# Kernel tuning notes

Hardware: AMD Instinct MI355X
Metric: run time of the kernel (lower is better)

## Reference

```python
import jax, jax.numpy as jnp
import numpy as np

N = 50000        # nodes
E = 1600000      # edges
G = 512          # graphs in batch
IN = 128         # in_dim
HID = 32         # hidden_dim
H = 4            # heads in conv1
NEG_SLOPE = 0.2  # PyG GATConv default


def setup_inputs() -> dict:
    key = jax.random.key(0)
    ks = jax.random.split(key, 20)
    s = 0.05
    return {
        "x": jax.random.normal(ks[0], (N, IN), jnp.float32),
        "edge_index": jax.random.randint(ks[1], (2, E), 0, N, dtype=jnp.int64),
        "edge_attr": jax.random.normal(ks[2], (E, 8), jnp.float32),
        "batch": jnp.sort(jax.random.randint(ks[3], (N,), 0, G, dtype=jnp.int64)),
        # conv1: in=IN, out=HID, heads=H, concat=True
        "W1": jax.random.normal(ks[4], (IN, H * HID), jnp.float32) * s,
        "a_src1": jax.random.normal(ks[5], (H, HID), jnp.float32) * s,
        "a_dst1": jax.random.normal(ks[6], (H, HID), jnp.float32) * s,
        "b1": jnp.zeros((H * HID,), jnp.float32),
        # conv2: in=H*HID, out=HID, heads=1, concat=False
        "W2": jax.random.normal(ks[7], (H * HID, HID), jnp.float32) * s,
        "a_src2": jax.random.normal(ks[8], (1, HID), jnp.float32) * s,
        "a_dst2": jax.random.normal(ks[9], (1, HID), jnp.float32) * s,
        "b2": jnp.zeros((HID,), jnp.float32),
        # classifier: HID -> HID//2 -> 1
        "Wc1": jax.random.normal(ks[10], (HID, HID // 2), jnp.float32) * s,
        "bc1": jnp.zeros((HID // 2,), jnp.float32),
        "Wc2": jax.random.normal(ks[11], (HID // 2, 1), jnp.float32) * s,
        "bc2": jnp.zeros((1,), jnp.float32),
    }


def gat_layer(x, src, dst, W, a_src, a_dst, b, heads, ch, concat, n):
    """PyG GATConv (eval mode): linear, edge-gathered additive attention,
    per-destination segment softmax, scatter-add aggregation."""
    h = (x @ W).reshape(n, heads, ch)                       # [N,H,C]
    alpha_s = jnp.sum(h * a_src, axis=-1)                   # [N,H]
    alpha_d = jnp.sum(h * a_dst, axis=-1)                   # [N,H]
    e = jax.nn.leaky_relu(alpha_s[src] + alpha_d[dst], NEG_SLOPE)  # [Etot,H]
    m = jax.lax.stop_gradient(jax.ops.segment_max(e, dst, num_segments=n))
    ex = jnp.exp(e - m[dst])
    den = jax.ops.segment_sum(ex, dst, num_segments=n)      # [N,H]
    alpha = ex / den[dst]                                   # [Etot,H]
    out = jax.ops.segment_sum(alpha[:, :, None] * h[src], dst, num_segments=n)
    out = out.reshape(n, heads * ch) if concat else out.mean(axis=1)
    return out + b


def reference(x, edge_index, edge_attr, batch,
              W1, a_src1, a_dst1, b1,
              W2, a_src2, a_dst2, b2,
              Wc1, bc1, Wc2, bc2):
    # add self-loops (PyG GATConv default)
    loop = jnp.arange(N, dtype=edge_index.dtype)
    src = jnp.concatenate([edge_index[0], loop])
    dst = jnp.concatenate([edge_index[1], loop])

    h = jax.nn.elu(gat_layer(x, src, dst, W1, a_src1, a_dst1, b1, H, HID, True, N))
    h = jax.nn.elu(gat_layer(h, src, dst, W2, a_src2, a_dst2, b2, 1, HID, False, N))

    # global mean pool over graphs
    cnt = jax.ops.segment_sum(jnp.ones((N,), h.dtype), batch, num_segments=G)
    pooled = jax.ops.segment_sum(h, batch, num_segments=G) / cnt[:, None]

    z = jax.nn.relu(pooled @ Wc1 + bc1)
    return (z @ Wc2 + bc2).squeeze(-1)   # [G]
```

## Files before the change

### kernel.cpp

```cpp
#include <hip/hip_runtime.h>
#include <math.h>

#define BUCKET_SHIFT 7
#define BUCKET_NODES (1 << BUCKET_SHIFT)
#define MAX_BUCK 512
#define PART_CHUNK 8192
#define PART_EPT 32

typedef _Float16 half4v __attribute__((ext_vector_type(4)));
typedef _Float16 half8v __attribute__((ext_vector_type(8)));

__device__ __forceinline__ float leaky02(float x){ return x > 0.f ? x : 0.2f * x; }
__device__ __forceinline__ float eluf(float x){ return x > 0.f ? x : expm1f(x); }

__global__ __launch_bounds__(128) void gemm1_kernel(
    const float* __restrict__ x, const float* __restrict__ W,
    const float* __restrict__ a_src, const float* __restrict__ a_dst,
    _Float16* __restrict__ h, float* __restrict__ as_, float* __restrict__ ad_, int n)
{
  const int t = threadIdx.x;
  const int row0 = blockIdx.x * 8;
  __shared__ float xs[8][128];
  __shared__ float sS[8][128];
  __shared__ float sD[8][128];
  for (int idx = t; idx < 8 * 32; idx += 128) {
    int r = idx >> 5, k4 = idx & 31;
    float4 v = (row0 + r < n) ? ((const float4*)x)[(size_t)(row0 + r) * 32 + k4]
                              : make_float4(0.f, 0.f, 0.f, 0.f);
    *(float4*)&xs[r][k4 * 4] = v;
  }
  __syncthreads();
  float acc[8] = {0,0,0,0,0,0,0,0};
  for (int k = 0; k < 128; k += 4) {
    float w0 = W[(k + 0) * 128 + t];
    float w1 = W[(k + 1) * 128 + t];
    float w2 = W[(k + 2) * 128 + t];
    float w3 = W[(k + 3) * 128 + t];
    #pragma unroll
    for (int r = 0; r < 8; ++r) {
      float4 xv = *(const float4*)&xs[r][k];
      acc[r] += xv.x * w0 + xv.y * w1 + xv.z * w2 + xv.w * w3;
    }
  }
  float asv = a_src[t], adv = a_dst[t];
  #pragma unroll
  for (int r = 0; r < 8; ++r) {
    float hv = acc[r];
    if (row0 + r < n) h[(size_t)(row0 + r) * 128 + t] = (_Float16)hv;
    sS[r][t] = hv * asv;
    sD[r][t] = hv * adv;
  }
  __syncthreads();
  if (t < 64) {
    int r = t >> 3, head = t & 3, which = (t >> 2) & 1;
    if (row0 + r < n) {
      const float (*buf)[128] = which ? sD : sS;
      double s = 0;
      for (int cc = 0; cc < 32; ++cc) s += (double)buf[r][head * 32 + cc];
      float* dstp = which ? ad_ : as_;
      dstp[(row0 + r) * 4 + head] = (float)s;
    }
  }
}

__global__ __launch_bounds__(128) void gemm2_kernel(
    const _Float16* __restrict__ x, const float* __restrict__ W,
    const float* __restrict__ a_src, const float* __restrict__ a_dst,
    _Float16* __restrict__ h, float* __restrict__ as_, float* __restrict__ ad_, int n)
{
  const int t = threadIdx.x;
  const int row0 = blockIdx.x * 8;
  __shared__ float xs[8][128];
  __shared__ float sH[8][32];
  for (int idx = t; idx < 8 * 16; idx += 128) {
    int r = idx >> 4, k8 = idx & 15;
    half8v v;
    #pragma unroll
    for (int q = 0; q < 8; ++q) v[q] = (_Float16)0.f;
    if (row0 + r < n) v = ((const half8v*)x)[(size_t)(row0 + r) * 16 + k8];
    #pragma unroll
    for (int q = 0; q < 8; ++q) xs[r][k8 * 8 + q] = (float)v[q];
  }
  __syncthreads();
  int col = t & 31, rp = t >> 5;
  int r0 = rp * 2, r1 = r0 + 1;
  float a0 = 0, a1 = 0;
  for (int k = 0; k < 128; k += 4) {
    float w0 = W[(k + 0) * 32 + col];
    float w1 = W[(k + 1) * 32 + col];
    float w2 = W[(k + 2) * 32 + col];
    float w3 = W[(k + 3) * 32 + col];
    float4 x0 = *(const float4*)&xs[r0][k];
    float4 x1 = *(const float4*)&xs[r1][k];
    a0 += x0.x * w0 + x0.y * w1 + x0.z * w2 + x0.w * w3;
    a1 += x1.x * w0 + x1.y * w1 + x1.z * w2 + x1.w * w3;
  }
  if (row0 + r0 < n) h[(size_t)(row0 + r0) * 32 + col] = (_Float16)a0;
  if (row0 + r1 < n) h[(size_t)(row0 + r1) * 32 + col] = (_Float16)a1;
  sH[r0][col] = a0; sH[r1][col] = a1;
  __syncthreads();
  if (t < 16) {
    int r = t >> 1, which = t & 1;
    if (row0 + r < n) {
      const float* a = which ? a_dst : a_src;
      double s = 0;
      for (int cc = 0; cc < 32; ++cc) s += (double)sH[r][cc] * (double)a[cc];
      (which ? ad_ : as_)[row0 + r] = (float)s;
    }
  }
}

__global__ __launch_bounds__(256) void bucket_hist_kernel(
    const int* __restrict__ dst, int* __restrict__ bucketCount, int E, int K)
{
  __shared__ int hist[MAX_BUCK];
  for (int b = threadIdx.x; b < K; b += 256) hist[b] = 0;
  __syncthreads();
  int cbase = blockIdx.x * PART_CHUNK;
  for (int j = 0; j < PART_EPT; ++j) {
    int e = cbase + j * 256 + threadIdx.x;
    if (e < E) atomicAdd(&hist[dst[e] >> BUCKET_SHIFT], 1);
  }
  __syncthreads();
  for (int b = threadIdx.x; b < K; b += 256)
    if (hist[b]) atomicAdd(&bucketCount[b], hist[b]);
}

__global__ __launch_bounds__(256) void partition_kernel(
    const int* __restrict__ src, const int* __restrict__ dst,
    const int* __restrict__ bucketStart, int* __restrict__ cursorB,
    int2* __restrict__ bucketed, int E, int K)
{
  __shared__ int hist[MAX_BUCK];
  __shared__ int base_s[MAX_BUCK];
  __shared__ int cur[MAX_BUCK];
  for (int b = threadIdx.x; b < K; b += 256) hist[b] = 0;
  __syncthreads();
  int cbase = blockIdx.x * PART_CHUNK;
  for (int j = 0; j < PART_EPT; ++j) {
    int e = cbase + j * 256 + threadIdx.x;
    if (e < E) atomicAdd(&hist[dst[e] >> BUCKET_SHIFT], 1);
  }
  __syncthreads();
  for (int b = threadIdx.x; b < K; b += 256) {
    int c = hist[b];
    base_s[b] = c ? bucketStart[b] + atomicAdd(&cursorB[b], c) : 0;
    cur[b] = 0;
  }
  __syncthreads();
  for (int j = 0; j < PART_EPT; ++j) {
    int e = cbase + j * 256 + threadIdx.x;
    if (e < E) {
      int d = dst[e];
      int b = d >> BUCKET_SHIFT;
      int r = atomicAdd(&cur[b], 1);
      bucketed[base_s[b] + r] = make_int2(src[e], d);
    }
  }
}

__global__ __launch_bounds__(256) void fill_csr_kernel(
    const int2* __restrict__ bucketed, const int* __restrict__ bucketStart,
    int* __restrict__ rowStart, int* __restrict__ col, int n, int E, int K)
{
  int b = blockIdx.x;
  int nodeBase = b << BUCKET_SHIFT;
  int t = threadIdx.x;
  __shared__ int hist[BUCKET_NODES];
  __shared__ int rs[BUCKET_NODES];
  __shared__ int cur[BUCKET_NODES];
  if (t < BUCKET_NODES) hist[t] = 0;
  __syncthreads();
  int bs = bucketStart[b];
  int be = (b + 1 < K) ? bucketStart[b + 1] : E;
  for (int i = bs + t; i < be; i += 256)
    atomicAdd(&hist[bucketed[i].y - nodeBase], 1);
  __syncthreads();
  if (t < BUCKET_NODES) rs[t] = hist[t];
  __syncthreads();
  for (int off = 1; off < BUCKET_NODES; off <<= 1) {
    int v = (t < BUCKET_NODES && t >= off) ? rs[t - off] : 0;
    __syncthreads();
    if (t < BUCKET_NODES) rs[t] += v;
    __syncthreads();
  }
  if (t < BUCKET_NODES) {
    int node = nodeBase + t;
    int excl = bs + rs[t] - hist[t];
    if (node < n) rowStart[node] = excl;
    rs[t] = excl;
    cur[t] = 0;
  }
  if (b == K - 1 && t == 0) rowStart[n] = E;
  __syncthreads();
  for (int i = bs + t; i < be; i += 256) {
    int2 rec = bucketed[i];
    int local = rec.y - nodeBase;
    int pos = rs[local] + atomicAdd(&cur[local], 1);
    col[pos] = rec.x;
  }
}

__global__ __launch_bounds__(256) void gat_aggr_w16_kernel(
    const _Float16* __restrict__ feat,
    const float* __restrict__ as_,
    const float* __restrict__ ad_,
    const int* __restrict__ rowStart,
    const int* __restrict__ col,
    const float* __restrict__ bias,
    _Float16* __restrict__ out, int n)
{
  constexpr int L    = 16;
  constexpr int NPW  = 4;
  constexpr int NPB  = 16;
  constexpr int CHUNK = 16;

  const int t    = threadIdx.x;
  const int wave = t >> 6;
  const int lane = t & 63;
  const int grp  = lane >> 4;
  const int li   = lane & 15;
  const int slot = wave * NPW + grp;
  const int node = blockIdx.x * NPB + slot;
  const int hc   = li >> 2;

  __shared__ int   s_off[NPB][CHUNK + 1];
  __shared__ float s_p[NPB][CHUNK * 4 + 1];

  if (node >= n) return;

  const int beg = rowStart[node];
  const int deg = rowStart[node + 1] - beg;

  const float4 advv = ((const float4*)ad_)[node];
  const float4 asvv = ((const float4*)as_)[node];
  float adv[4] = {advv.x, advv.y, advv.z, advv.w};
  float eself[4];
  eself[0] = leaky02(asvv.x + adv[0]);
  eself[1] = leaky02(asvv.y + adv[1]);
  eself[2] = leaky02(asvv.z + adv[2]);
  eself[3] = leaky02(asvv.w + adv[3]);
  float es = 0.f;
  #pragma unroll
  for (int h = 0; h < 4; ++h) if (h == hc) es = eself[h];
  const float ps = expf(es);

  const char* featc = (const char*)feat + (li << 4);
  const half8v fself = *(const half8v*)(featc + ((size_t)node << 8));
  double acc64[8];
  #pragma unroll
  for (int q = 0; q < 8; ++q) acc64[q] = (double)ps * (double)(float)fself[q];
  double den64 = (double)ps;

  for (int base = 0; base < deg; base += CHUNK) {
    const int cnt = min(CHUNK, deg - base);
    if (li < cnt) {
      int s = col[beg + base + li];
      s_off[slot][li] = s << 8;
      float4 q = ((const float4*)as_)[s];
      s_p[slot][li * 4 + 0] = expf(leaky02(q.x + adv[0]));
      s_p[slot][li * 4 + 1] = expf(leaky02(q.y + adv[1]));
      s_p[slot][li * 4 + 2] = expf(leaky02(q.z + adv[2]));
      s_p[slot][li * 4 + 3] = expf(leaky02(q.w + adv[3]));
    }
    __builtin_amdgcn_wave_barrier();
    float a[8] = {0,0,0,0,0,0,0,0};
    float df = 0.f;
    #pragma unroll 4
    for (int j = 0; j < cnt; ++j) {
      int boff = s_off[slot][j];
      float p = s_p[slot][j * 4 + hc];
      const half8v f = *(const half8v*)(featc + boff);
      #pragma unroll
      for (int q = 0; q < 8; ++q) a[q] += p * (float)f[q];
      df += p;
    }
    __builtin_amdgcn_wave_barrier();
    #pragma unroll
    for (int q = 0; q < 8; ++q) acc64[q] += a[q];
    den64 += df;
  }

  const float4 bv0 = ((const float4*)bias)[2 * li];
  const float4 bv1 = ((const float4*)bias)[2 * li + 1];
  const float bb[8] = {bv0.x, bv0.y, bv0.z, bv0.w, bv1.x, bv1.y, bv1.z, bv1.w};
  const double inv = 1.0 / den64;
  half8v ov;
  #pragma unroll
  for (int q = 0; q < 8; ++q)
    ov[q] = (_Float16)eluf((float)(acc64[q] * inv) + bb[q]);
  *(half8v*)((char*)out + ((size_t)node << 8) + (li << 4)) = ov;
}

template<int CTOT, int H>
__global__ __launch_bounds__(256) void gat_aggr3_kernel(
    const _Float16* __restrict__ feat,
    const float* __restrict__ as_,
    const float* __restrict__ ad_,
    const int* __restrict__ rowStart,
    const int* __restrict__ col,
    const float* __restrict__ bias,
    float* __restrict__ out, int n)
{
  constexpr int L    = CTOT / 4;
  constexpr int NPW  = 64 / L;
  constexpr int NPB  = 4 * NPW;
  constexpr int CH   = CTOT / H;
  constexpr int CHUNK = L;

  const int t    = threadIdx.x;
  const int wave = t >> 6;
  const int lane = t & 63;
  const int grp  = lane / L;
  const int li   = lane % L;
  const int slot = wave * NPW + grp;
  const int node = blockIdx.x * NPB + slot;
  const int hc   = (4 * li) / CH;

  __shared__ int   s_off[NPB][CHUNK + 1];
  __shared__ float s_p[NPB][CHUNK * H + 1];

  if (node >= n) return;

  const int beg = rowStart[node];
  const int deg = rowStart[node + 1] - beg;

  float adv[H], eself[H];
  #pragma unroll
  for (int h = 0; h < H; ++h) adv[h] = ad_[node * H + h];
  #pragma unroll
  for (int h = 0; h < H; ++h) eself[h] = leaky02(as_[node * H + h] + adv[h]);

  float es = 0.f;
  #pragma unroll
  for (int h = 0; h < H; ++h) if (h == hc) es = eself[h];
  const float ps = expf(es);

  const half4v fself = *(const half4v*)(feat + (size_t)node * CTOT + 4 * li);
  double acc64[4];
  acc64[0] = (double)ps * (double)(float)fself.x;
  acc64[1] = (double)ps * (double)(float)fself.y;
  acc64[2] = (double)ps * (double)(float)fself.z;
  acc64[3] = (double)ps * (double)(float)fself.w;
  double den64 = (double)ps;

  for (int base = 0; base < deg; base += CHUNK) {
    const int cnt = min(CHUNK, deg - base);
    if (li < cnt) {
      int s = col[beg + base + li];
      s_off[slot][li] = s * CTOT;
      if constexpr (H == 4) {
        float4 q = ((const float4*)as_)[s];
        s_p[slot][li * 4 + 0] = expf(leaky02(q.x + adv[0]));
        s_p[slot][li * 4 + 1] = expf(leaky02(q.y + adv[1]));
        s_p[slot][li * 4 + 2] = expf(leaky02(q.z + adv[2]));
        s_p[slot][li * 4 + 3] = expf(leaky02(q.w + adv[3]));
      } else {
        s_p[slot][li] = expf(leaky02(as_[s] + adv[0]));
      }
    }
    __builtin_amdgcn_wave_barrier();
    float a0 = 0.f, a1 = 0.f, a2 = 0.f, a3 = 0.f, df = 0.f;
    #pragma unroll 8
    for (int j = 0; j < cnt; ++j) {
      int off = s_off[slot][j];
      float p = (H == 4) ? s_p[slot][j * 4 + hc] : s_p[slot][j];
      const half4v f = *(const half4v*)(feat + off + 4 * li);
      a0 += p * (float)f.x; a1 += p * (float)f.y;
      a2 += p * (float)f.z; a3 += p * (float)f.w;
      df += p;
    }
    __builtin_amdgcn_wave_barrier();
    acc64[0] += a0; acc64[1] += a1; acc64[2] += a2; acc64[3] += a3;
    den64 += df;
  }

  const float4 bv = *(const float4*)(bias + 4 * li);
  float4 o;
  o.x = eluf((float)(acc64[0] / den64) + bv.x);
  o.y = eluf((float)(acc64[1] / den64) + bv.y);
  o.z = eluf((float)(acc64[2] / den64) + bv.z);
  o.w = eluf((float)(acc64[3] / den64) + bv.w);
  *(float4*)(out + (size_t)node * CTOT + 4 * li) = o;
}

__global__ __launch_bounds__(256) void pool_kernel(const float* __restrict__ act2,
    const int* __restrict__ batch, float* __restrict__ pooled,
    float* __restrict__ cnt, int n)
{
  int t = threadIdx.x;
  int c = t & 31, r = t >> 5;
  int n0 = blockIdx.x * 64 + r * 8;
  float run = 0.f; int gcur = -1; int len = 0;
  for (int i = 0; i < 8; ++i) {
    int nd = n0 + i;
    if (nd >= n) break;
    int gb = batch[nd];
    if (gb != gcur) {
      if (gcur >= 0) {
        atomicAdd(&pooled[gcur * 32 + c], run);
        if (c == 0) atomicAdd(&cnt[gcur], (float)len);
      }
      gcur = gb; run = 0.f; len = 0;
    }
    run += act2[(size_t)nd * 32 + c];
    len++;
  }
  if (gcur >= 0) {
    atomicAdd(&pooled[gcur * 32 + c], run);
    if (c == 0) atomicAdd(&cnt[gcur], (float)len);
  }
}

__global__ void classifier_kernel(const float* __restrict__ pooled, const float* __restrict__ cnt,
    const float* __restrict__ Wc1, const float* __restrict__ bc1,
    const float* __restrict__ Wc2, const float* __restrict__ bc2,
    float* __restrict__ outp, int g_total)
{
  int g = blockIdx.x * blockDim.x + threadIdx.x;
  if (g < g_total) {
    float inv = 1.0f / cnt[g];
    float pm[32];
    for (int c = 0; c < 32; ++c) pm[c] = pooled[g * 32 + c] * inv;
    double o = (double)bc2[0];
    for (int j = 0; j < 16; ++j) {
      double z = (double)bc1[j];
      for (int c = 0; c < 32; ++c) z += (double)pm[c] * (double)Wc1[c * 16 + j];
      float zr = (float)z;
      zr = zr > 0.f ? zr : 0.f;
      o += (double)zr * (double)Wc2[j];
    }
    outp[g] = (float)o;
  }
}

extern "C" void kernel_launch(void* const* d_in, const int* in_sizes, int n_in,
                              void* d_out, int out_size, void* d_ws, size_t ws_size,
                              hipStream_t stream)
{
  const float* x      = (const float*)d_in[0];
  const int*   ei     = (const int*)d_in[1];
  const int*   batch  = (const int*)d_in[3];
  const float* W1     = (const float*)d_in[4];
  const float* a_src1 = (const float*)d_in[5];
  const float* a_dst1 = (const float*)d_in[6];
  const float* b1     = (const float*)d_in[7];
  const float* W2     = (const float*)d_in[8];
  const float* a_src2 = (const float*)d_in[9];
  const float* a_dst2 = (const float*)d_in[10];
  const float* b2     = (const float*)d_in[11];
  const float* Wc1    = (const float*)d_in[12];
  const float* bc1    = (const float*)d_in[13];
  const float* Wc2    = (const float*)d_in[14];
  const float* bc2    = (const float*)d_in[15];

  const int N = in_sizes[0] / 128;
  const int E = in_sizes[1] / 2;
  const int G = out_size;

  const int* srcv = ei;
  const int* dstv = ei + E;

  char* ws = (char*)d_ws;
  size_t off = 0;
  auto alloc = [&](size_t bytes) -> void* {
    void* p = ws + off;
    off += (bytes + 255) & ~(size_t)255;
    return p;
  };
  _Float16* h1   = (_Float16*)alloc((size_t)N * 128 * 2);
  _Float16* act1 = (_Float16*)alloc((size_t)N * 128 * 2);
  _Float16* h2   = (_Float16*)alloc((size_t)N * 32 * 2);
  float* act2  = (float*)alloc((size_t)N * 32 * 4);
  float* as1   = (float*)alloc((size_t)N * 4 * 4);
  float* ad1   = (float*)alloc((size_t)N * 4 * 4);
  float* as2   = (float*)alloc((size_t)N * 4);
  float* ad2   = (float*)alloc((size_t)N * 4);
  int*   rowStart = (int*)alloc((size_t)(N + 1) * 4);
  int*   colv     = (int*)alloc((size_t)E * 4);
  int*   bucketCount = (int*)alloc((size_t)MAX_BUCK * 4);
  int*   cursorB     = (int*)alloc((size_t)MAX_BUCK * 4);
  int2*  bucketed    = (int2*)alloc((size_t)E * 8);
  float* pooled   = (float*)alloc((size_t)G * 32 * 4);
  float* cntG     = (float*)alloc((size_t)G * 4);

  const int K = (N + BUCKET_NODES - 1) >> BUCKET_SHIFT;

  hipMemsetAsync(bucketCount, 0, (size_t)K * 4, stream);
  hipMemsetAsync(cursorB,     0, (size_t)K * 4, stream);
  hipMemsetAsync(pooled, 0, (size_t)G * 32 * 4, stream);
  hipMemsetAsync(cntG,   0, (size_t)G * 4, stream);

  int pb = (E + PART_CHUNK - 1) / PART_CHUNK;
  bucket_hist_kernel<<<pb, 256, 0, stream>>>(dstv, bucketCount, E, K);
  {
    extern __global__ void scan_offsets_kernel(int*, int);
  }
  void(0);
  {
    extern const int __dummy;
  }
  extern __global__ void scan_offsets_kernel(int* __restrict__, int);
  scan_offsets_kernel<<<1, 256, 0, stream>>>(bucketCount, K);
  partition_kernel<<<pb, 256, 0, stream>>>(srcv, dstv, bucketCount, cursorB, bucketed, E, K);
  fill_csr_kernel<<<K, 256, 0, stream>>>(bucketed, bucketCount, rowStart, colv, N, E, K);

  gemm1_kernel<<<(N + 7) / 8, 128, 0, stream>>>(x, W1, a_src1, a_dst1, h1, as1, ad1, N);
  gat_aggr_w16_kernel<<<(N + 15) / 16, 256, 0, stream>>>(h1, as1, ad1, rowStart, colv, b1, act1, N);

  gemm2_kernel<<<(N + 7) / 8, 128, 0, stream>>>(act1, W2, a_src2, a_dst2, h2, as2, ad2, N);
  gat_aggr3_kernel<32, 1><<<(N + 31) / 32, 256, 0, stream>>>(h2, as2, ad2, rowStart, colv, b2, act2, N);

  pool_kernel<<<(N + 63) / 64, 256, 0, stream>>>(act2, batch, pooled, cntG, N);
  classifier_kernel<<<(G + 255) / 256, 256, 0, stream>>>(pooled, cntG, Wc1, bc1, Wc2, bc2,
                                                         (float*)d_out, G);
}

__global__ __launch_bounds__(256) void scan_offsets_kernel(int* __restrict__ partial, int nb) {
  __shared__ int s[256];
  __shared__ int carry_s;
  int t = threadIdx.x;
  if (t == 0) carry_s = 0;
  __syncthreads();
  for (int b = 0; b < nb; b += 256) {
    int v = (b + t < nb) ? partial[b + t] : 0;
    s[t] = v;
    __syncthreads();
    for (int off = 1; off < 256; off <<= 1) {
      int x = (t >= off) ? s[t - off] : 0;
      __syncthreads();
      s[t] += x;
      __syncthreads();
    }
    int incl = s[t];
    int carry = carry_s;
    if (b + t < nb) partial[b + t] = carry + incl - v;
    __syncthreads();
    if (t == 255) carry_s = carry + incl;
    __syncthreads();
  }
}
```

Measured before the change: 398.3 us.

## Fuse setup launches, pack bucketed edges, prefetch and batch gathers in aggregation

Four memsets are replaced by zeroing inside gemm1's first block. The offset scan is folded into bucket_hist through a last-block-done counter, and the classifier is folded into the pool kernel the same way. Bucketed edge records shrink from int2 to one packed 32-bit word (src<<7 | local dst), which halves the partition and fill traffic. Both aggregation kernels now prefetch the next chunk's column indices and source scores one chunk ahead, and issue all 16 feature gathers before accumulating. Risks are the ordering assumption that gemm1 finishes zeroing before bucket_hist starts (same stream), higher register pressure from 16 outstanding loads, and the packed encoding requiring src < 2^25.

```diff
diff --git a/kernel.cpp b/kernel.cpp
--- a/kernel.cpp
+++ b/kernel.cpp
@@ -16,9 +16,13 @@
 __global__ __launch_bounds__(128) void gemm1_kernel(
     const float* __restrict__ x, const float* __restrict__ W,
     const float* __restrict__ a_src, const float* __restrict__ a_dst,
-    _Float16* __restrict__ h, float* __restrict__ as_, float* __restrict__ ad_, int n)
+    _Float16* __restrict__ h, float* __restrict__ as_, float* __restrict__ ad_, int n,
+    int* __restrict__ zbase, int zwords)
 {
   const int t = threadIdx.x;
+  if (blockIdx.x == 0) {
+    for (int i = t; i < zwords; i += 128) zbase[i] = 0;
+  }
   const int row0 = blockIdx.x * 8;
   __shared__ float xs[8][128];
   __shared__ float sS[8][128];
@@ -111,25 +115,53 @@
 }
 
 __global__ __launch_bounds__(256) void bucket_hist_kernel(
-    const int* __restrict__ dst, int* __restrict__ bucketCount, int E, int K)
+    const int* __restrict__ dst, int* __restrict__ bucketCount,
+    int* __restrict__ doneCtr, int E, int K)
 {
   __shared__ int hist[MAX_BUCK];
-  for (int b = threadIdx.x; b < K; b += 256) hist[b] = 0;
+  const int t = threadIdx.x;
+  for (int b = t; b < K; b += 256) hist[b] = 0;
   __syncthreads();
   int cbase = blockIdx.x * PART_CHUNK;
   for (int j = 0; j < PART_EPT; ++j) {
-    int e = cbase + j * 256 + threadIdx.x;
+    int e = cbase + j * 256 + t;
     if (e < E) atomicAdd(&hist[dst[e] >> BUCKET_SHIFT], 1);
   }
   __syncthreads();
-  for (int b = threadIdx.x; b < K; b += 256)
+  for (int b = t; b < K; b += 256)
     if (hist[b]) atomicAdd(&bucketCount[b], hist[b]);
+  __threadfence();
+  __shared__ unsigned int tick;
+  if (t == 0) tick = atomicAdd((unsigned int*)doneCtr, 1u);
+  __syncthreads();
+  if (tick != gridDim.x - 1) return;
+  __shared__ int s[256];
+  __shared__ int carry_s;
+  if (t == 0) carry_s = 0;
+  __syncthreads();
+  for (int b = 0; b < K; b += 256) {
+    int v = (b + t < K) ? atomicAdd(&bucketCount[b + t], 0) : 0;
+    s[t] = v;
+    __syncthreads();
+    for (int off = 1; off < 256; off <<= 1) {
+      int x = (t >= off) ? s[t - off] : 0;
+      __syncthreads();
+      s[t] += x;
+      __syncthreads();
+    }
+    int incl = s[t];
+    int carry = carry_s;
+    if (b + t < K) bucketCount[b + t] = carry + incl - v;
+    __syncthreads();
+    if (t == 255) carry_s = carry + incl;
+    __syncthreads();
+  }
 }
 
 __global__ __launch_bounds__(256) void partition_kernel(
     const int* __restrict__ src, const int* __restrict__ dst,
     const int* __restrict__ bucketStart, int* __restrict__ cursorB,
-    int2* __restrict__ bucketed, int E, int K)
+    unsigned int* __restrict__ bucketed, int E, int K)
 {
   __shared__ int hist[MAX_BUCK];
   __shared__ int base_s[MAX_BUCK];
@@ -154,13 +186,14 @@
       int d = dst[e];
       int b = d >> BUCKET_SHIFT;
       int r = atomicAdd(&cur[b], 1);
-      bucketed[base_s[b] + r] = make_int2(src[e], d);
+      bucketed[base_s[b] + r] =
+          ((unsigned int)src[e] << BUCKET_SHIFT) | (unsigned int)(d & (BUCKET_NODES - 1));
     }
   }
 }
 
 __global__ __launch_bounds__(256) void fill_csr_kernel(
-    const int2* __restrict__ bucketed, const int* __restrict__ bucketStart,
+    const unsigned int* __restrict__ bucketed, const int* __restrict__ bucketStart,
     int* __restrict__ rowStart, int* __restrict__ col, int n, int E, int K)
 {
   int b = blockIdx.x;
@@ -174,7 +207,7 @@
   int bs = bucketStart[b];
   int be = (b + 1 < K) ? bucketStart[b + 1] : E;
   for (int i = bs + t; i < be; i += 256)
-    atomicAdd(&hist[bucketed[i].y - nodeBase], 1);
+    atomicAdd(&hist[bucketed[i] & (BUCKET_NODES - 1)], 1);
   __syncthreads();
   if (t < BUCKET_NODES) rs[t] = hist[t];
   __syncthreads();
@@ -194,14 +227,14 @@
   if (b == K - 1 && t == 0) rowStart[n] = E;
   __syncthreads();
   for (int i = bs + t; i < be; i += 256) {
-    int2 rec = bucketed[i];
-    int local = rec.y - nodeBase;
+    unsigned int rec = bucketed[i];
+    int local = rec & (BUCKET_NODES - 1);
     int pos = rs[local] + atomicAdd(&cur[local], 1);
-    col[pos] = rec.x;
-  }
-}
-
-__global__ __launch_bounds__(256) void gat_aggr_w16_kernel(
+    col[pos] = (int)(rec >> BUCKET_SHIFT);
+  }
+}
+
+__global__ __launch_bounds__(256) void gat_aggr1_kernel(
     const _Float16* __restrict__ feat,
     const float* __restrict__ as_,
     const float* __restrict__ ad_,
@@ -210,22 +243,18 @@
     const float* __restrict__ bias,
     _Float16* __restrict__ out, int n)
 {
-  constexpr int L    = 16;
-  constexpr int NPW  = 4;
-  constexpr int NPB  = 16;
   constexpr int CHUNK = 16;
-
   const int t    = threadIdx.x;
   const int wave = t >> 6;
   const int lane = t & 63;
   const int grp  = lane >> 4;
   const int li   = lane & 15;
-  const int slot = wave * NPW + grp;
-  const int node = blockIdx.x * NPB + slot;
+  const int slot = wave * 4 + grp;
+  const int node = blockIdx.x * 16 + slot;
   const int hc   = li >> 2;
 
-  __shared__ int   s_off[NPB][CHUNK + 1];
-  __shared__ float s_p[NPB][CHUNK * 4 + 1];
+  __shared__ int   s_off[16][CHUNK];
+  __shared__ float s_p[16][CHUNK * 4];
 
   if (node >= n) return;
 
@@ -234,15 +263,15 @@
 
   const float4 advv = ((const float4*)ad_)[node];
   const float4 asvv = ((const float4*)as_)[node];
-  float adv[4] = {advv.x, advv.y, advv.z, advv.w};
-  float eself[4];
-  eself[0] = leaky02(asvv.x + adv[0]);
-  eself[1] = leaky02(asvv.y + adv[1]);
-  eself[2] = leaky02(asvv.z + adv[2]);
-  eself[3] = leaky02(asvv.w + adv[3]);
-  float es = 0.f;
-  #pragma unroll
-  for (int h = 0; h < 4; ++h) if (h == hc) es = eself[h];
+  const float adv[4] = {advv.x, advv.y, advv.z, advv.w};
+  float es;
+  {
+    float e0 = leaky02(asvv.x + adv[0]);
+    float e1 = leaky02(asvv.y + adv[1]);
+    float e2 = leaky02(asvv.z + adv[2]);
+    float e3 = leaky02(asvv.w + adv[3]);
+    es = (hc == 0) ? e0 : (hc == 1) ? e1 : (hc == 2) ? e2 : e3;
+  }
   const float ps = expf(es);
 
   const char* featc = (const char*)feat + (li << 4);
@@ -252,28 +281,57 @@
   for (int q = 0; q < 8; ++q) acc64[q] = (double)ps * (double)(float)fself[q];
   double den64 = (double)ps;
 
-  for (int base = 0; base < deg; base += CHUNK) {
-    const int cnt = min(CHUNK, deg - base);
+  int    st_s = 0;
+  float4 st_q = make_float4(0.f, 0.f, 0.f, 0.f);
+  if (deg > 0 && li < min(CHUNK, deg)) {
+    st_s = col[beg + li];
+    st_q = ((const float4*)as_)[st_s];
+  }
+
+  const int nch = (deg + CHUNK - 1) / CHUNK;
+  for (int c = 0; c < nch; ++c) {
+    const int base = c * CHUNK;
+    const int cnt  = min(CHUNK, deg - base);
     if (li < cnt) {
-      int s = col[beg + base + li];
-      s_off[slot][li] = s << 8;
-      float4 q = ((const float4*)as_)[s];
-      s_p[slot][li * 4 + 0] = expf(leaky02(q.x + adv[0]));
-      s_p[slot][li * 4 + 1] = expf(leaky02(q.y + adv[1]));
-      s_p[slot][li * 4 + 2] = expf(leaky02(q.z + adv[2]));
-      s_p[slot][li * 4 + 3] = expf(leaky02(q.w + adv[3]));
+      s_off[slot][li] = st_s << 8;
+      float4 pp;
+      pp.x = expf(leaky02(st_q.x + adv[0]));
+      pp.y = expf(leaky02(st_q.y + adv[1]));
+      pp.z = expf(leaky02(st_q.z + adv[2]));
+      pp.w = expf(leaky02(st_q.w + adv[3]));
+      *(float4*)&s_p[slot][li * 4] = pp;
     }
     __builtin_amdgcn_wave_barrier();
+    const int nbase = base + CHUNK;
+    if (nbase + li < deg) {
+      st_s = col[beg + nbase + li];
+      st_q = ((const float4*)as_)[st_s];
+    }
     float a[8] = {0,0,0,0,0,0,0,0};
     float df = 0.f;
-    #pragma unroll 4
-    for (int j = 0; j < cnt; ++j) {
-      int boff = s_off[slot][j];
-      float p = s_p[slot][j * 4 + hc];
-      const half8v f = *(const half8v*)(featc + boff);
+    if (cnt == CHUNK) {
+      int off[16];
       #pragma unroll
-      for (int q = 0; q < 8; ++q) a[q] += p * (float)f[q];
-      df += p;
+      for (int j = 0; j < 16; ++j) off[j] = s_off[slot][j];
+      half8v r[16];
+      #pragma unroll
+      for (int j = 0; j < 16; ++j) r[j] = *(const half8v*)(featc + off[j]);
+      #pragma unroll
+      for (int j = 0; j < 16; ++j) {
+        float p = s_p[slot][j * 4 + hc];
+        #pragma unroll
+        for (int q = 0; q < 8; ++q) a[q] += p * (float)r[j][q];
+        df += p;
+      }
+    } else {
+      for (int j = 0; j < cnt; ++j) {
+        int off = s_off[slot][j];
+        float p = s_p[slot][j * 4 + hc];
+        const half8v f = *(const half8v*)(featc + off);
+        #pragma unroll
+        for (int q = 0; q < 8; ++q) a[q] += p * (float)f[q];
+        df += p;
+      }
     }
     __builtin_amdgcn_wave_barrier();
     #pragma unroll
@@ -292,8 +350,7 @@
   *(half8v*)((char*)out + ((size_t)node << 8) + (li << 4)) = ov;
 }
 
-template<int CTOT, int H>
-__global__ __launch_bounds__(256) void gat_aggr3_kernel(
+__global__ __launch_bounds__(256) void gat_aggr2_kernel(
     const _Float16* __restrict__ feat,
     const float* __restrict__ as_,
     const float* __restrict__ ad_,
@@ -302,41 +359,28 @@
     const float* __restrict__ bias,
     float* __restrict__ out, int n)
 {
-  constexpr int L    = CTOT / 4;
-  constexpr int NPW  = 64 / L;
-  constexpr int NPB  = 4 * NPW;
-  constexpr int CH   = CTOT / H;
-  constexpr int CHUNK = L;
-
+  constexpr int CHUNK = 16;
   const int t    = threadIdx.x;
   const int wave = t >> 6;
   const int lane = t & 63;
-  const int grp  = lane / L;
-  const int li   = lane % L;
-  const int slot = wave * NPW + grp;
-  const int node = blockIdx.x * NPB + slot;
-  const int hc   = (4 * li) / CH;
-
-  __shared__ int   s_off[NPB][CHUNK + 1];
-  __shared__ float s_p[NPB][CHUNK * H + 1];
+  const int grp  = lane >> 3;
+  const int li   = lane & 7;
+  const int slot = wave * 8 + grp;
+  const int node = blockIdx.x * 32 + slot;
+
+  __shared__ int   s_off[32][CHUNK];
+  __shared__ float s_p[32][CHUNK];
 
   if (node >= n) return;
 
   const int beg = rowStart[node];
   const int deg = rowStart[node + 1] - beg;
 
-  float adv[H], eself[H];
-  #pragma unroll
-  for (int h = 0; h < H; ++h) adv[h] = ad_[node * H + h];
-  #pragma unroll
-  for (int h = 0; h < H; ++h) eself[h] = leaky02(as_[node * H + h] + adv[h]);
-
-  float es = 0.f;
-  #pragma unroll
-  for (int h = 0; h < H; ++h) if (h == hc) es = eself[h];
-  const float ps = expf(es);
-
-  const half4v fself = *(const half4v*)(feat + (size_t)node * CTOT + 4 * li);
+  const float adv = ad_[node];
+  const float ps  = expf(leaky02(as_[node] + adv));
+
+  const char* featc = (const char*)feat + (li << 3);
+  const half4v fself = *(const half4v*)(featc + ((size_t)node << 6));
   double acc64[4];
   acc64[0] = (double)ps * (double)(float)fself.x;
   acc64[1] = (double)ps * (double)(float)fself.y;
@@ -344,49 +388,73 @@
   acc64[3] = (double)ps * (double)(float)fself.w;
   double den64 = (double)ps;
 
-  for (int base = 0; base < deg; base += CHUNK) {
-    const int cnt = min(CHUNK, deg - base);
-    if (li < cnt) {
-      int s = col[beg + base + li];
-      s_off[slot][li] = s * CTOT;
-      if constexpr (H == 4) {
-        float4 q = ((const float4*)as_)[s];
-        s_p[slot][li * 4 + 0] = expf(leaky02(q.x + adv[0]));
-        s_p[slot][li * 4 + 1] = expf(leaky02(q.y + adv[1]));
-        s_p[slot][li * 4 + 2] = expf(leaky02(q.z + adv[2]));
-        s_p[slot][li * 4 + 3] = expf(leaky02(q.w + adv[3]));
-      } else {
-        s_p[slot][li] = expf(leaky02(as_[s] + adv[0]));
+  int   st_s0 = 0, st_s1 = 0;
+  float st_q0 = 0.f, st_q1 = 0.f;
+  if (deg > 0) {
+    int c0 = min(CHUNK, deg);
+    if (li < c0)     { st_s0 = col[beg + li];     st_q0 = as_[st_s0]; }
+    if (li + 8 < c0) { st_s1 = col[beg + li + 8]; st_q1 = as_[st_s1]; }
+  }
+
+  const int nch = (deg + CHUNK - 1) / CHUNK;
+  for (int c = 0; c < nch; ++c) {
+    const int base = c * CHUNK;
+    const int cnt  = min(CHUNK, deg - base);
+    if (li < cnt)     { s_off[slot][li]     = st_s0 << 6; s_p[slot][li]     = expf(leaky02(st_q0 + adv)); }
+    if (li + 8 < cnt) { s_off[slot][li + 8] = st_s1 << 6; s_p[slot][li + 8] = expf(leaky02(st_q1 + adv)); }
+    __builtin_amdgcn_wave_barrier();
+    const int nbase = base + CHUNK;
+    if (nbase < deg) {
+      if (nbase + li < deg)     { st_s0 = col[beg + nbase + li];     st_q0 = as_[st_s0]; }
+      if (nbase + li + 8 < deg) { st_s1 = col[beg + nbase + li + 8]; st_q1 = as_[st_s1]; }
+    }
+    float a0 = 0.f, a1 = 0.f, a2 = 0.f, a3 = 0.f, df = 0.f;
+    if (cnt == CHUNK) {
+      int off[16];
+      #pragma unroll
+      for (int j = 0; j < 16; ++j) off[j] = s_off[slot][j];
+      half4v r[16];
+      #pragma unroll
+      for (int j = 0; j < 16; ++j) r[j] = *(const half4v*)(featc + off[j]);
+      #pragma unroll
+      for (int j = 0; j < 16; ++j) {
+        float p = s_p[slot][j];
+        a0 += p * (float)r[j].x; a1 += p * (float)r[j].y;
+        a2 += p * (float)r[j].z; a3 += p * (float)r[j].w;
+        df += p;
       }
-    }
-    __builtin_amdgcn_wave_barrier();
-    float a0 = 0.f, a1 = 0.f, a2 = 0.f, a3 = 0.f, df = 0.f;
-    #pragma unroll 8
-    for (int j = 0; j < cnt; ++j) {
-      int off = s_off[slot][j];
-      float p = (H == 4) ? s_p[slot][j * 4 + hc] : s_p[slot][j];
-      const half4v f = *(const half4v*)(feat + off + 4 * li);
-      a0 += p * (float)f.x; a1 += p * (float)f.y;
-      a2 += p * (float)f.z; a3 += p * (float)f.w;
-      df += p;
+    } else {
+      for (int j = 0; j < cnt; ++j) {
+        int off = s_off[slot][j];
+        float p = s_p[slot][j];
+        const half4v f = *(const half4v*)(featc + off);
+        a0 += p * (float)f.x; a1 += p * (float)f.y;
+        a2 += p * (float)f.z; a3 += p * (float)f.w;
+        df += p;
+      }
     }
     __builtin_amdgcn_wave_barrier();
     acc64[0] += a0; acc64[1] += a1; acc64[2] += a2; acc64[3] += a3;
     den64 += df;
   }
 
+  const double inv = 1.0 / den64;
   const float4 bv = *(const float4*)(bias + 4 * li);
   float4 o;
-  o.x = eluf((float)(acc64[0] / den64) + bv.x);
-  o.y = eluf((float)(acc64[1] / den64) + bv.y);
-  o.z = eluf((float)(acc64[2] / den64) + bv.z);
-  o.w = eluf((float)(acc64[3] / den64) + bv.w);
-  *(float4*)(out + (size_t)node * CTOT + 4 * li) = o;
-}
-
-__global__ __launch_bounds__(256) void pool_kernel(const float* __restrict__ act2,
-    const int* __restrict__ batch, float* __restrict__ pooled,
-    float* __restrict__ cnt, int n)
+  o.x = eluf((float)(acc64[0] * inv) + bv.x);
+  o.y = eluf((float)(acc64[1] * inv) + bv.y);
+  o.z = eluf((float)(acc64[2] * inv) + bv.z);
+  o.w = eluf((float)(acc64[3] * inv) + bv.w);
+  *(float4*)(out + (size_t)node * 32 + 4 * li) = o;
+}
+
+__global__ __launch_bounds__(256) void pool_classify_kernel(
+    const float* __restrict__ act2, const int* __restrict__ batch,
+    float* __restrict__ pooled, float* __restrict__ cnt, int n,
+    int* __restrict__ poolCtr,
+    const float* __restrict__ Wc1, const float* __restrict__ bc1,
+    const float* __restrict__ Wc2, const float* __restrict__ bc2,
+    float* __restrict__ outp, int G)
 {
   int t = threadIdx.x;
   int c = t & 31, r = t >> 5;
@@ -410,22 +478,20 @@
     atomicAdd(&pooled[gcur * 32 + c], run);
     if (c == 0) atomicAdd(&cnt[gcur], (float)len);
   }
-}
-
-__global__ void classifier_kernel(const float* __restrict__ pooled, const float* __restrict__ cnt,
-    const float* __restrict__ Wc1, const float* __restrict__ bc1,
-    const float* __restrict__ Wc2, const float* __restrict__ bc2,
-    float* __restrict__ outp, int g_total)
-{
-  int g = blockIdx.x * blockDim.x + threadIdx.x;
-  if (g < g_total) {
-    float inv = 1.0f / cnt[g];
+  __threadfence();
+  __shared__ unsigned int tick;
+  if (t == 0) tick = atomicAdd((unsigned int*)poolCtr, 1u);
+  __syncthreads();
+  if (tick != gridDim.x - 1) return;
+  for (int g = t; g < G; g += 256) {
+    float cg = atomicAdd(&cnt[g], 0.f);
+    float inv = 1.0f / cg;
     float pm[32];
-    for (int c = 0; c < 32; ++c) pm[c] = pooled[g * 32 + c] * inv;
+    for (int cc = 0; cc < 32; ++cc) pm[cc] = atomicAdd(&pooled[g * 32 + cc], 0.f) * inv;
     double o = (double)bc2[0];
     for (int j = 0; j < 16; ++j) {
       double z = (double)bc1[j];
-      for (int c = 0; c < 32; ++c) z += (double)pm[c] * (double)Wc1[c * 16 + j];
+      for (int cc = 0; cc < 32; ++cc) z += (double)pm[cc] * (double)Wc1[cc * 16 + j];
       float zr = (float)z;
       zr = zr > 0.f ? zr : 0.f;
       o += (double)zr * (double)Wc2[j];
@@ -478,65 +544,32 @@
   float* ad2   = (float*)alloc((size_t)N * 4);
   int*   rowStart = (int*)alloc((size_t)(N + 1) * 4);
   int*   colv     = (int*)alloc((size_t)E * 4);
+  unsigned int* bucketed = (unsigned int*)alloc((size_t)E * 4);
+  size_t zoff0 = off;
   int*   bucketCount = (int*)alloc((size_t)MAX_BUCK * 4);
   int*   cursorB     = (int*)alloc((size_t)MAX_BUCK * 4);
-  int2*  bucketed    = (int2*)alloc((size_t)E * 8);
-  float* pooled   = (float*)alloc((size_t)G * 32 * 4);
-  float* cntG     = (float*)alloc((size_t)G * 4);
+  int*   ctrs        = (int*)alloc(8);
+  float* pooled      = (float*)alloc((size_t)G * 32 * 4);
+  float* cntG        = (float*)alloc((size_t)G * 4);
+  size_t zoff1 = off;
+  const int zwords = (int)((zoff1 - zoff0) / 4);
+  int* zbase = bucketCount;
 
   const int K = (N + BUCKET_NODES - 1) >> BUCKET_SHIFT;
-
-  hipMemsetAsync(bucketCount, 0, (size_t)K * 4, stream);
-  hipMemsetAsync(cursorB,     0, (size_t)K * 4, stream);
-  hipMemsetAsync(pooled, 0, (size_t)G * 32 * 4, stream);
-  hipMemsetAsync(cntG,   0, (size_t)G * 4, stream);
-
-  int pb = (E + PART_CHUNK - 1) / PART_CHUNK;
-  bucket_hist_kernel<<<pb, 256, 0, stream>>>(dstv, bucketCount, E, K);
-  {
-    extern __global__ void scan_offsets_kernel(int*, int);
-  }
-  void(0);
-  {
-    extern const int __dummy;
-  }
-  extern __global__ void scan_offsets_kernel(int* __restrict__, int);
-  scan_offsets_kernel<<<1, 256, 0, stream>>>(bucketCount, K);
+  const int pb = (E + PART_CHUNK - 1) / PART_CHUNK;
+
+  gemm1_kernel<<<(N + 7) / 8, 128, 0, stream>>>(x, W1, a_src1, a_dst1, h1, as1, ad1, N,
+                                                zbase, zwords);
+  bucket_hist_kernel<<<pb, 256, 0, stream>>>(dstv, bucketCount, &ctrs[0], E, K);
   partition_kernel<<<pb, 256, 0, stream>>>(srcv, dstv, bucketCount, cursorB, bucketed, E, K);
   fill_csr_kernel<<<K, 256, 0, stream>>>(bucketed, bucketCount, rowStart, colv, N, E, K);
 
-  gemm1_kernel<<<(N + 7) / 8, 128, 0, stream>>>(x, W1, a_src1, a_dst1, h1, as1, ad1, N);
-  gat_aggr_w16_kernel<<<(N + 15) / 16, 256, 0, stream>>>(h1, as1, ad1, rowStart, colv, b1, act1, N);
+  gat_aggr1_kernel<<<(N + 15) / 16, 256, 0, stream>>>(h1, as1, ad1, rowStart, colv, b1, act1, N);
 
   gemm2_kernel<<<(N + 7) / 8, 128, 0, stream>>>(act1, W2, a_src2, a_dst2, h2, as2, ad2, N);
-  gat_aggr3_kernel<32, 1><<<(N + 31) / 32, 256, 0, stream>>>(h2, as2, ad2, rowStart, colv, b2, act2, N);
-
-  pool_kernel<<<(N + 63) / 64, 256, 0, stream>>>(act2, batch, pooled, cntG, N);
-  classifier_kernel<<<(G + 255) / 256, 256, 0, stream>>>(pooled, cntG, Wc1, bc1, Wc2, bc2,
-                                                         (float*)d_out, G);
-}
-
-__global__ __launch_bounds__(256) void scan_offsets_kernel(int* __restrict__ partial, int nb) {
-  __shared__ int s[256];
-  __shared__ int carry_s;
-  int t = threadIdx.x;
-  if (t == 0) carry_s = 0;
-  __syncthreads();
-  for (int b = 0; b < nb; b += 256) {
-    int v = (b + t < nb) ? partial[b + t] : 0;
-    s[t] = v;
-    __syncthreads();
-    for (int off = 1; off < 256; off <<= 1) {
-      int x = (t >= off) ? s[t - off] : 0;
-      __syncthreads();
-      s[t] += x;
-      __syncthreads();
-    }
-    int incl = s[t];
-    int carry = carry_s;
-    if (b + t < nb) partial[b + t] = carry + incl - v;
-    __syncthreads();
-    if (t == 255) carry_s = carry + incl;
-    __syncthreads();
-  }
-}
+  gat_aggr2_kernel<<<(N + 31) / 32, 256, 0, stream>>>(h2, as2, ad2, rowStart, colv, b2, act2, N);
+
+  pool_classify_kernel<<<(N + 63) / 64, 256, 0, stream>>>(act2, batch, pooled, cntG, N,
+                                                          &ctrs[1], Wc1, bc1, Wc2, bc2,
+                                                          (float*)d_out, G);
+}
```

New measurement: 465.7 us. +16.9%, slower.
